# Kernel optimization log

Hardware: AMD Instinct MI355X
Metric: run time of the kernel (lower is better)

## Reference

```python
import jax, jax.numpy as jnp
import numpy as np

B_, H_, N_, L_ = 4, 512, 64, 2048  # batch, d_model, d_state/2 (conj pairs), seq len


def setup_inputs() -> dict:
    key = jax.random.key(0)
    ks = jax.random.split(key, 8)
    x = jax.random.normal(ks[0], (B_, H_, L_), jnp.float32)
    ln_w = jnp.ones((H_,), jnp.float32)
    ln_b = jnp.zeros((H_,), jnp.float32)
    # S4D-style init: dt log-uniform in [1e-3, 1e-1], A = -1/2 + i*pi*n (S4D-Lin)
    log_dt = jax.random.uniform(ks[1], (H_,), jnp.float32) * (np.log(0.1) - np.log(0.001)) + np.log(0.001)
    log_A_real = jnp.broadcast_to(jnp.log(jnp.float32(0.5)), (H_, N_))
    A_imag = jnp.broadcast_to(np.pi * jnp.arange(N_, dtype=np.float32), (H_, N_))
    B_re = jnp.ones((H_, N_), jnp.float32)
    B_im = jnp.zeros((H_, N_), jnp.float32)
    # 2 kernel channels for bidirectional
    C_re = jax.random.normal(ks[2], (2, H_, N_), jnp.float32) * (0.5 ** 0.5)
    C_im = jax.random.normal(ks[3], (2, H_, N_), jnp.float32) * (0.5 ** 0.5)
    D = jax.random.normal(ks[4], (H_,), jnp.float32)
    W_out = jax.random.normal(ks[5], (H_, H_), jnp.float32) / np.sqrt(H_)
    b_out = jnp.zeros((H_,), jnp.float32)
    return dict(x=x, ln_w=ln_w, ln_b=ln_b, log_dt=log_dt, log_A_real=log_A_real,
                A_imag=A_imag, B_re=B_re, B_im=B_im, C_re=C_re, C_im=C_im,
                D=D, W_out=W_out, b_out=b_out)


def _s4_layer(x, ln_w, ln_b, log_dt, log_A_real, A_imag, B_re, B_im, C_re, C_im, D, W_out, b_out):
    Bb, H, L = x.shape
    # ---- pre-norm LayerNorm over channel dim (module transposes to (B,L,H)) ----
    zt = x.transpose(0, 2, 1)                          # (B, L, H)
    mu = zt.mean(-1, keepdims=True)
    var = jnp.mean((zt - mu) ** 2, -1, keepdims=True)
    zt = (zt - mu) * jax.lax.rsqrt(var + 1e-5) * ln_w + ln_b
    z = zt.transpose(0, 2, 1)                          # (B, H, L)
    # ---- S4 diagonal SSM kernel, ZOH discretization, 2 channels (bidirectional) ----
    dt = jnp.exp(log_dt)[:, None]                      # (H, 1)
    A = -jnp.exp(log_A_real) + 1j * A_imag             # (H, N)
    dtA = A * dt                                       # (H, N)
    dB = (B_re + 1j * B_im) * (jnp.exp(dtA) - 1.0) / A # (H, N) discretized B
    CB = (C_re + 1j * C_im) * dB                       # (2, H, N)
    V = jnp.exp(dtA[:, :, None] * jnp.arange(L))       # (H, N, L) Vandermonde exp(l*dt*A)
    k = 2.0 * jnp.real(jnp.einsum('chn,hnl->chl', CB, V))  # (2, H, L)
    # ---- bidirectional: causal + flipped anticausal kernel, length 2L ----
    zpad = jnp.zeros_like(k[0])
    kb = jnp.concatenate([k[0], zpad], -1) + jnp.concatenate([zpad, k[1][:, ::-1]], -1)  # (H, 2L)
    # ---- FFT convolution ----
    k_f = jnp.fft.rfft(kb, n=2 * L)                    # (H, L+1)
    u_f = jnp.fft.rfft(z, n=2 * L)                     # (B, H, L+1)
    y = jnp.fft.irfft(u_f * k_f, n=2 * L)[..., :L]     # (B, H, L)
    y = y + z * D[:, None]                             # skip connection D*u
    y = jax.nn.gelu(y)                                 # default S4 activation
    y = jnp.einsum('oh,bhl->bol', W_out, y) + b_out[:, None]  # output linear (Conv1d k=1)
    return y + x                                       # residual of S4Layer


def reference(x, ln_w, ln_b, log_dt, log_A_real, A_imag, B_re, B_im, C_re, C_im, D, W_out, b_out):
    return _s4_layer(x, ln_w, ln_b, log_dt, log_A_real, A_imag, B_re, B_im, C_re, C_im, D, W_out, b_out)
```

## Files before the change

### kernel.cpp

```cpp
#include <hip/hip_runtime.h>
#include <math.h>

#define Bq 4
#define Hq 512
#define Nq 64
#define Lq 2048
#define PARAM (Hq*Nq)
#define T 64
#define NC (Lq/T)
#define NCOL 256

__global__ void prep_kernel(const float* __restrict__ log_dt,
                            const float* __restrict__ log_A_real,
                            const float* __restrict__ A_imag,
                            const float* __restrict__ B_re, const float* __restrict__ B_im,
                            const float* __restrict__ C_re, const float* __restrict__ C_im,
                            float* __restrict__ a0, float* __restrict__ b0,
                            float* __restrict__ a1, float* __restrict__ b1,
                            float* __restrict__ pw, float* __restrict__ pwT) {
    int idx = blockIdx.x * blockDim.x + threadIdx.x;
    if (idx >= PARAM) return;
    int h = idx >> 6, n = idx & 63;
    float dt = expf(log_dt[h]);
    float Ar = -expf(log_A_real[idx]);
    float Ai = A_imag[idx];
    float er = expf(Ar * dt);
    float wr = er * cosf(Ai * dt);
    float wi = er * sinf(Ai * dt);
    float mr = wr - 1.0f, mi = wi;
    float den = Ar * Ar + Ai * Ai;
    float qr = (mr * Ar + mi * Ai) / den;
    float qi = (mi * Ar - mr * Ai) / den;
    float Br = B_re[idx], Bi = B_im[idx];
    float dBr = Br * qr - Bi * qi;
    float dBi = Br * qi + Bi * qr;
    float cr = C_re[idx], ci = C_im[idx];
    a0[idx] =  2.0f * (cr * dBr - ci * dBi);
    b0[idx] = -2.0f * (cr * dBi + ci * dBr);
    cr = C_re[PARAM + idx]; ci = C_im[PARAM + idx];
    a1[idx] =  2.0f * (cr * dBr - ci * dBi);
    b1[idx] = -2.0f * (cr * dBi + ci * dBr);
    float c = 1.f, s = 0.f;
    float* base  = pw  + (size_t)h * 65 * 128 + 2 * n;
    float* baseT = pwT + (size_t)(h * 64 + n) * 132;
    for (int d = 0; d <= 64; ++d) {
        *(float2*)(base + (size_t)d * 128) = float2{c, s};
        *(float2*)(baseT + 2 * d)          = float2{c, s};
        float nc = c * wr - s * wi;
        float ns = c * wi + s * wr;
        c = nc; s = ns;
    }
}

__global__ __launch_bounds__(128)
void ktap_kernel(const float* __restrict__ pw,
                 const float* __restrict__ a0, const float* __restrict__ b0,
                 const float* __restrict__ a1, const float* __restrict__ b1,
                 float* __restrict__ kt) {
    int h = blockIdx.x;
    int t = threadIdx.x;
    int dir = t >> 6, d = t & 63;
    const float* aa = dir ? a1 : a0;
    const float* bb = dir ? b1 : b0;
    const float* row = pw + (size_t)(h * 65 + d) * 128;
    float acc = 0.f;
    for (int n = 0; n < 64; ++n) {
        float2 v = *(const float2*)(row + 2 * n);
        acc = fmaf(aa[h * 64 + n], v.x, acc);
        acc = fmaf(bb[h * 64 + n], v.y, acc);
    }
    kt[((size_t)h * 2 + dir) * 64 + d] = acc;
}

__global__ __launch_bounds__(256)
void ln_kernel(const float* __restrict__ x, const float* __restrict__ lnw,
               const float* __restrict__ lnb, float* __restrict__ z) {
    int blk = blockIdx.x;
    int b  = blk / (Lq / 16);
    int l0 = (blk % (Lq / 16)) * 16;
    int tx = threadIdx.x & 15;
    int ty = threadIdx.x >> 4;
    const float* xb = x + (size_t)b * Hq * Lq;
    float s = 0.f, s2 = 0.f;
    for (int h = ty; h < Hq; h += 16) {
        float v = xb[h * Lq + l0 + tx];
        s += v; s2 += v * v;
    }
    __shared__ float rs_[16][17], r2_[16][17], mu_s[16], sg_s[16];
    rs_[ty][tx] = s; r2_[ty][tx] = s2;
    __syncthreads();
    if (ty == 0) {
        float a = 0.f, c = 0.f;
        #pragma unroll
        for (int i = 0; i < 16; ++i) { a += rs_[i][tx]; c += r2_[i][tx]; }
        float mu = a * (1.0f / Hq);
        float var = c * (1.0f / Hq) - mu * mu;
        mu_s[tx] = mu;
        sg_s[tx] = rsqrtf(var + 1e-5f);
    }
    __syncthreads();
    float mu = mu_s[tx], rs = sg_s[tx];
    float* zb = z + (size_t)b * Hq * Lq;
    for (int h = ty; h < Hq; h += 16) {
        float v = xb[h * Lq + l0 + tx];
        zb[h * Lq + l0 + tx] = (v - mu) * rs * lnw[h] + lnb[h];
    }
}

__global__ __launch_bounds__(256, 6)
void delta_kernel(const float* __restrict__ z, const float* __restrict__ pw,
                  float* __restrict__ buf) {
    __shared__ float Bs[64][68];
    int h = blockIdx.x, ct = blockIdx.y;
    int t = threadIdx.x;
    int dir = ct >> 1;
    int cc = t & 31, rb = (t >> 5) & 1, jg = t >> 6;
    int b = (ct & 1) * 2 + rb;
    const float* zb = z + ((size_t)b * Hq + h) * Lq;
    if (dir == 0) {
        #pragma unroll
        for (int f = 0; f < 4; ++f) {
            float4 v = *(const float4*)(zb + cc * 64 + 16 * jg + 4 * f);
            Bs[16*jg+4*f+0][rb*32+cc] = v.x;
            Bs[16*jg+4*f+1][rb*32+cc] = v.y;
            Bs[16*jg+4*f+2][rb*32+cc] = v.z;
            Bs[16*jg+4*f+3][rb*32+cc] = v.w;
        }
    } else {
        #pragma unroll
        for (int f = 0; f < 4; ++f) {
            float4 v = *(const float4*)(zb + 2044 - cc * 64 - 16 * jg - 4 * f);
            Bs[16*jg+4*f+3][rb*32+cc] = v.x;
            Bs[16*jg+4*f+2][rb*32+cc] = v.y;
            Bs[16*jg+4*f+1][rb*32+cc] = v.z;
            Bs[16*jg+4*f+0][rb*32+cc] = v.w;
        }
    }
    __syncthreads();
    int tx = t & 15, ty = t >> 4;
    float aR[4][4] = {}, aI[4][4] = {};
    const float* pwh = pw + (size_t)h * 65 * 128;
    #pragma unroll 4
    for (int kk = 0; kk < 64; ++kk) {
        int d = 63 - kk;
        const float4* pr = (const float4*)(pwh + (size_t)d * 128 + 8 * tx);
        float4 p0 = pr[0], p1 = pr[1];
        float4 bv = *(const float4*)&Bs[kk][4 * ty];
        float pc[4] = {p0.x, p0.z, p1.x, p1.z};
        float ps[4] = {p0.y, p0.w, p1.y, p1.w};
        #pragma unroll
        for (int rr = 0; rr < 4; ++rr) {
            #pragma unroll
            for (int q = 0; q < 4; ++q) {
                aR[rr][q] = fmaf(pc[rr], (&bv.x)[q], aR[rr][q]);
                aI[rr][q] = fmaf(ps[rr], (&bv.x)[q], aI[rr][q]);
            }
        }
    }
    #pragma unroll
    for (int q = 0; q < 4; ++q) {
        int colg = ct * 64 + 4 * ty + q;
        float* dst = buf + ((size_t)h * NCOL + colg) * 128 + 8 * tx;
        float4 v1, v2;
        v1.x = aR[0][q]; v1.y = aI[0][q]; v1.z = aR[1][q]; v1.w = aI[1][q];
        v2.x = aR[2][q]; v2.y = aI[2][q]; v2.z = aR[3][q]; v2.w = aI[3][q];
        *(float4*)dst = v1; *(float4*)(dst + 4) = v2;
    }
}

__global__ __launch_bounds__(256)
void cscan_kernel(const float* __restrict__ pw, float* __restrict__ buf) {
    int e = blockIdx.x * 4 + (threadIdx.x >> 6);
    int n = threadIdx.x & 63;
    int h = e >> 3, dir = (e >> 2) & 1, b = e & 3;
    float2 t64 = *(const float2*)(pw + (size_t)(h * 65 + 64) * 128 + 2 * n);
    float tc = t64.x, ts = t64.y;
    float sr = 0.f, si = 0.f;
    float2* p = (float2*)(buf + ((size_t)h * NCOL + dir * 128 + b * 32) * 128) + n;
    float2 d = p[0];
    for (int c = 0; c < NC; ++c) {
        float2 dn;
        if (c + 1 < NC) dn = p[(c + 1) * 64];
        float2 s; s.x = sr; s.y = si;
        p[c * 64] = s;
        float nr = fmaf(tc, sr, fmaf(-ts, si, d.x));
        float ni = fmaf(ts, sr, fmaf(tc, si, d.y));
        sr = nr; si = ni; d = dn;
    }
}

__global__ __launch_bounds__(256, 4)
void yact_kernel(const float* __restrict__ z, const float* __restrict__ pwT,
                 const float* __restrict__ a0, const float* __restrict__ b0,
                 const float* __restrict__ a1, const float* __restrict__ b1,
                 const float* __restrict__ kt, const float* __restrict__ buf,
                 const float* __restrict__ Dv, float* __restrict__ u) {
    __shared__ float As[64][68];
    __shared__ float Bs[64][68];
    __shared__ float ks0[64], ks1[64], as0_[64], bs0_[64], as1_[64], bs1_[64];
    int h = blockIdx.x, bp = blockIdx.y;
    int t = threadIdx.x;
    if (t < 64) {
        ks0[t]  = kt[((size_t)h * 2 + 0) * 64 + t];
        ks1[t]  = kt[((size_t)h * 2 + 1) * 64 + t];
        as0_[t] = a0[h * 64 + t]; bs0_[t] = b0[h * 64 + t];
        as1_[t] = a1[h * 64 + t]; bs1_[t] = b1[h * 64 + t];
    }
    int tx = t & 15, ty = t >> 4;
    int si = t & 63, kg = t >> 6;
    int bS = 2 * bp + (si >> 5), ch = si & 31;
    const float* zb   = z + ((size_t)bS * Hq + h) * Lq + ch * 64;
    const float* bufh = buf + (size_t)h * NCOL * 128;
    const float* buf0 = bufh + (size_t)(bS * 32 + ch) * 128;
    const float* buf1 = bufh + (size_t)(128 + bS * 32 + (31 - ch)) * 128;
    const float* pwh  = pwT + (size_t)h * 64 * 132;
    float4 rB[4];
    float2 pv[8];
    #pragma unroll
    for (int f = 0; f < 4; ++f)
        rB[f] = *(const float4*)(zb + 16 * kg + 4 * f);
    float acc[4][4] = {};
    __syncthreads();
    for (int p = 0; p < 5; ++p) {
        if (p == 0) {
            #pragma unroll
            for (int q = 0; q < 16; ++q) {
                int kk = 16 * kg + q;
                int d = si - kk;
                As[kk][si] = (d >= 0) ? ks0[d] : ks1[-d - 1];
            }
        } else {
            const float* as_ = (p < 3) ? as0_ : as1_;
            const float* bs_ = (p < 3) ? bs0_ : bs1_;
            int pp = (p < 3) ? (p - 1) : (p - 3);
            #pragma unroll
            for (int q = 0; q < 16; ++q) {
                int j = q >> 1;
                int n = 32 * pp + 8 * kg + j;
                float vx = pv[j].x, vy = pv[j].y;
                As[16 * kg + q][si] = ((q & 1) == 0)
                    ? fmaf(as_[n], vx, bs_[n] * vy)
                    : fmaf(bs_[n], vx, -as_[n] * vy);
            }
        }
        #pragma unroll
        for (int f = 0; f < 4; ++f) {
            Bs[16*kg + 4*f + 0][si] = rB[f].x;
            Bs[16*kg + 4*f + 1][si] = rB[f].y;
            Bs[16*kg + 4*f + 2][si] = rB[f].z;
            Bs[16*kg + 4*f + 3][si] = rB[f].w;
        }
        __syncthreads();
        if (p < 4) {
            int pn = p + 1;
            int pp = (pn < 3) ? (pn - 1) : (pn - 3);
            const float* src = (pn < 3) ? buf0 : buf1;
            #pragma unroll
            for (int f = 0; f < 4; ++f)
                rB[f] = *(const float4*)(src + 64 * pp + 16 * kg + 4 * f);
            int dsel = (pn < 3) ? (si + 1) : (63 - si);
            #pragma unroll
            for (int j = 0; j < 8; ++j) {
                int n = 32 * pp + 8 * kg + j;
                pv[j] = *(const float2*)(pwh + (size_t)n * 132 + 2 * dsel);
            }
        }
        #pragma unroll 8
        for (int kk = 0; kk < 64; ++kk) {
            float4 av = *(const float4*)&As[kk][4 * tx];
            float4 bv = *(const float4*)&Bs[kk][4 * ty];
            #pragma unroll
            for (int ii = 0; ii < 4; ++ii) {
                float a = (&av.x)[ii];
                acc[ii][0] = fmaf(a, bv.x, acc[ii][0]);
                acc[ii][1] = fmaf(a, bv.y, acc[ii][1]);
                acc[ii][2] = fmaf(a, bv.z, acc[ii][2]);
                acc[ii][3] = fmaf(a, bv.w, acc[ii][3]);
            }
        }
        __syncthreads();
    }
    float dv = Dv[h];
    #pragma unroll
    for (int q = 0; q < 4; ++q) {
        int cc2 = 4 * ty + q;
        int b2 = 2 * bp + (cc2 >> 5), ch2 = cc2 & 31;
        size_t base = ((size_t)b2 * Hq + h) * Lq + ch2 * 64 + 4 * tx;
        float4 zr = *(const float4*)(z + base);
        float vv[4];
        vv[0] = acc[0][q] + dv * zr.x;
        vv[1] = acc[1][q] + dv * zr.y;
        vv[2] = acc[2][q] + dv * zr.z;
        vv[3] = acc[3][q] + dv * zr.w;
        #pragma unroll
        for (int i = 0; i < 4; ++i) {
            float v = vv[i];
            float tt = tanhf(0.7978845608028654f * (v + 0.044715f * v * v * v));
            vv[i] = 0.5f * v * (1.0f + tt);
        }
        float4 r; r.x = vv[0]; r.y = vv[1]; r.z = vv[2]; r.w = vv[3];
        *(float4*)(u + base) = r;
    }
}

__global__ __launch_bounds__(512, 4)
void gemm_kernel(const float* __restrict__ u, const float* __restrict__ W,
                 const float* __restrict__ bias, const float* __restrict__ x,
                 float* __restrict__ out) {
    int l0 = blockIdx.x * 64;
    int o0 = blockIdx.y * 128;
    int b  = blockIdx.z;
    int tid = threadIdx.x;
    __shared__ float Ws[2][32][132];
    __shared__ float Us[2][32][68];
    const float* ub = u + (size_t)b * Hq * Lq;
    float acc[4][4] = {};
    int wo = tid >> 4, wl = tid & 15;
    int sj = tid & 31, so = tid >> 5;
    int sl = tid & 63, sk = tid >> 6;
    float wreg[8], ureg[4];
    #pragma unroll
    for (int r = 0; r < 8; ++r) wreg[r] = W[(size_t)(o0 + so + 16*r) * Hq + sj];
    #pragma unroll
    for (int r = 0; r < 4; ++r) ureg[r] = ub[(size_t)(4*sk + r) * Lq + l0 + sl];
    #pragma unroll
    for (int r = 0; r < 8; ++r) Ws[0][sj][so + 16*r] = wreg[r];
    #pragma unroll
    for (int r = 0; r < 4; ++r) Us[0][4*sk + r][sl] = ureg[r];
    __syncthreads();
    for (int t = 0; t < Hq / 32; ++t) {
        int cur = t & 1;
        if (t < 15) {
            int k0 = (t + 1) * 32;
            #pragma unroll
            for (int r = 0; r < 8; ++r)
                wreg[r] = W[(size_t)(o0 + so + 16*r) * Hq + k0 + sj];
            #pragma unroll
            for (int r = 0; r < 4; ++r)
                ureg[r] = ub[(size_t)(k0 + 4*sk + r) * Lq + l0 + sl];
        }
        #pragma unroll 8
        for (int j = 0; j < 32; ++j) {
            float4 av = *(const float4*)&Ws[cur][j][4 * wo];
            float4 bv = *(const float4*)&Us[cur][j][4 * wl];
            #pragma unroll
            for (int io = 0; io < 4; ++io) {
                float a = (&av.x)[io];
                acc[io][0] = fmaf(a, bv.x, acc[io][0]);
                acc[io][1] = fmaf(a, bv.y, acc[io][1]);
                acc[io][2] = fmaf(a, bv.z, acc[io][2]);
                acc[io][3] = fmaf(a, bv.w, acc[io][3]);
            }
        }
        if (t < 15) {
            int nxt = cur ^ 1;
            #pragma unroll
            for (int r = 0; r < 8; ++r) Ws[nxt][sj][so + 16*r] = wreg[r];
            #pragma unroll
            for (int r = 0; r < 4; ++r) Us[nxt][4*sk + r][sl] = ureg[r];
        }
        __syncthreads();
    }
    #pragma unroll
    for (int io = 0; io < 4; ++io) {
        int o = o0 + 4 * wo + io;
        float bo = bias[o];
        size_t base = ((size_t)b * Hq + o) * Lq + l0 + 4 * wl;
        const float4 xr = *(const float4*)(x + base);
        float4 r;
        r.x = acc[io][0] + bo + xr.x;
        r.y = acc[io][1] + bo + xr.y;
        r.z = acc[io][2] + bo + xr.z;
        r.w = acc[io][3] + bo + xr.w;
        *(float4*)(out + base) = r;
    }
}

extern "C" void kernel_launch(void* const* d_in, const int* in_sizes, int n_in,
                              void* d_out, int out_size, void* d_ws, size_t ws_size,
                              hipStream_t stream) {
    (void)in_sizes; (void)n_in; (void)out_size; (void)ws_size;
    const float* x          = (const float*)d_in[0];
    const float* ln_w       = (const float*)d_in[1];
    const float* ln_b       = (const float*)d_in[2];
    const float* log_dt     = (const float*)d_in[3];
    const float* log_A_real = (const float*)d_in[4];
    const float* A_imag     = (const float*)d_in[5];
    const float* B_re       = (const float*)d_in[6];
    const float* B_im       = (const float*)d_in[7];
    const float* C_re       = (const float*)d_in[8];
    const float* C_im       = (const float*)d_in[9];
    const float* Dv         = (const float*)d_in[10];
    const float* W          = (const float*)d_in[11];
    const float* b_out      = (const float*)d_in[12];
    float* out = (float*)d_out;
    float* ws  = (float*)d_ws;

    const size_t BHL = (size_t)Bq * Hq * Lq;
    float* a0  = ws;
    float* b0  = ws + (size_t)PARAM;
    float* a1  = ws + 2 * (size_t)PARAM;
    float* b1  = ws + 3 * (size_t)PARAM;
    float* kt  = ws + 4 * (size_t)PARAM;
    float* pw  = ws + 6 * (size_t)PARAM;
    float* pwT = ws + 136 * (size_t)PARAM;
    float* z   = ws + 268 * (size_t)PARAM;
    float* u   = z  + BHL;
    float* buf = u + BHL;

    prep_kernel<<<PARAM / 256, 256, 0, stream>>>(log_dt, log_A_real, A_imag,
                                                 B_re, B_im, C_re, C_im,
                                                 a0, b0, a1, b1, pw, pwT);
    ln_kernel<<<Bq * (Lq / 16), 256, 0, stream>>>(x, ln_w, ln_b, z);
    ktap_kernel<<<Hq, 128, 0, stream>>>(pw, a0, b0, a1, b1, kt);
    delta_kernel<<<dim3(Hq, 4), 256, 0, stream>>>(z, pw, buf);
    cscan_kernel<<<Bq * Hq * 2 / 4, 256, 0, stream>>>(pw, buf);
    yact_kernel<<<dim3(Hq, 2), 256, 0, stream>>>(z, pwT, a0, b0, a1, b1,
                                                 kt, buf, Dv, u);
    gemm_kernel<<<dim3(Lq / 64, Hq / 128, Bq), 512, 0, stream>>>(u, W, b_out, x, out);
}
```

Baseline: 316.3 us.

## Restructure output GEMM to read W via wave-uniform scalar loads

The output projection GEMM changes from a 128x64 tile with both W and u staged in shared memory to a 32x128 tile where each wave owns 8 output rows. W values are wave-uniform, read through readfirstlane-indexed loads, which the compiler can turn into scalar loads, so only u is double-buffered in LDS. This removes the W shared-memory traffic and the transpose stores, at the cost of lower per-thread reuse (8x2 accumulators instead of 4x4) and more blocks.

```diff
diff --git a/kernel.cpp b/kernel.cpp
--- a/kernel.cpp
+++ b/kernel.cpp
@@ -303,76 +303,75 @@
     }
 }
 
-__global__ __launch_bounds__(512, 4)
+__global__ __launch_bounds__(256, 4)
 void gemm_kernel(const float* __restrict__ u, const float* __restrict__ W,
                  const float* __restrict__ bias, const float* __restrict__ x,
                  float* __restrict__ out) {
-    int l0 = blockIdx.x * 64;
-    int o0 = blockIdx.y * 128;
+    __shared__ float Us[2][32][128];
+    int l0 = blockIdx.x * 128;
+    int o0 = blockIdx.y * 32;
     int b  = blockIdx.z;
-    int tid = threadIdx.x;
-    __shared__ float Ws[2][32][132];
-    __shared__ float Us[2][32][68];
+    int t  = threadIdx.x;
+    int wv = __builtin_amdgcn_readfirstlane(t >> 6);
+    int ln = t & 63;
+    int ow = o0 + 8 * wv;
     const float* ub = u + (size_t)b * Hq * Lq;
-    float acc[4][4] = {};
-    int wo = tid >> 4, wl = tid & 15;
-    int sj = tid & 31, so = tid >> 5;
-    int sl = tid & 63, sk = tid >> 6;
-    float wreg[8], ureg[4];
-    #pragma unroll
-    for (int r = 0; r < 8; ++r) wreg[r] = W[(size_t)(o0 + so + 16*r) * Hq + sj];
-    #pragma unroll
-    for (int r = 0; r < 4; ++r) ureg[r] = ub[(size_t)(4*sk + r) * Lq + l0 + sl];
-    #pragma unroll
-    for (int r = 0; r < 8; ++r) Ws[0][sj][so + 16*r] = wreg[r];
-    #pragma unroll
-    for (int r = 0; r < 4; ++r) Us[0][4*sk + r][sl] = ureg[r];
+    int sf = t & 31;
+    int sk = t >> 5;
+    float4 st[4];
+    #pragma unroll
+    for (int r = 0; r < 4; ++r)
+        st[r] = *(const float4*)(ub + (size_t)(sk + 8*r) * Lq + l0 + 4*sf);
+    #pragma unroll
+    for (int r = 0; r < 4; ++r)
+        *(float4*)&Us[0][sk + 8*r][4*sf] = st[r];
     __syncthreads();
-    for (int t = 0; t < Hq / 32; ++t) {
-        int cur = t & 1;
-        if (t < 15) {
-            int k0 = (t + 1) * 32;
-            #pragma unroll
-            for (int r = 0; r < 8; ++r)
-                wreg[r] = W[(size_t)(o0 + so + 16*r) * Hq + k0 + sj];
+    float acc[8][2] = {};
+    for (int kt = 0; kt < Hq / 32; ++kt) {
+        int cur = kt & 1;
+        if (kt < 15) {
+            int k0 = (kt + 1) * 32;
             #pragma unroll
             for (int r = 0; r < 4; ++r)
-                ureg[r] = ub[(size_t)(k0 + 4*sk + r) * Lq + l0 + sl];
-        }
-        #pragma unroll 8
-        for (int j = 0; j < 32; ++j) {
-            float4 av = *(const float4*)&Ws[cur][j][4 * wo];
-            float4 bv = *(const float4*)&Us[cur][j][4 * wl];
-            #pragma unroll
-            for (int io = 0; io < 4; ++io) {
-                float a = (&av.x)[io];
-                acc[io][0] = fmaf(a, bv.x, acc[io][0]);
-                acc[io][1] = fmaf(a, bv.y, acc[io][1]);
-                acc[io][2] = fmaf(a, bv.z, acc[io][2]);
-                acc[io][3] = fmaf(a, bv.w, acc[io][3]);
-            }
-        }
-        if (t < 15) {
+                st[r] = *(const float4*)(ub + (size_t)(k0 + sk + 8*r) * Lq + l0 + 4*sf);
+        }
+        #pragma unroll
+        for (int ks = 0; ks < 4; ++ks) {
+            float ws[8][8];
+            #pragma unroll
+            for (int o = 0; o < 8; ++o) {
+                const float* wrow = W + (size_t)(ow + o) * Hq + kt * 32 + ks * 8;
+                #pragma unroll
+                for (int kk = 0; kk < 8; ++kk) ws[o][kk] = wrow[kk];
+            }
+            #pragma unroll
+            for (int kk = 0; kk < 8; ++kk) {
+                float2 uv = *(const float2*)&Us[cur][ks * 8 + kk][2 * ln];
+                #pragma unroll
+                for (int o = 0; o < 8; ++o) {
+                    acc[o][0] = fmaf(ws[o][kk], uv.x, acc[o][0]);
+                    acc[o][1] = fmaf(ws[o][kk], uv.y, acc[o][1]);
+                }
+            }
+        }
+        if (kt < 15) {
             int nxt = cur ^ 1;
             #pragma unroll
-            for (int r = 0; r < 8; ++r) Ws[nxt][sj][so + 16*r] = wreg[r];
-            #pragma unroll
-            for (int r = 0; r < 4; ++r) Us[nxt][4*sk + r][sl] = ureg[r];
+            for (int r = 0; r < 4; ++r)
+                *(float4*)&Us[nxt][sk + 8*r][4*sf] = st[r];
         }
         __syncthreads();
     }
     #pragma unroll
-    for (int io = 0; io < 4; ++io) {
-        int o = o0 + 4 * wo + io;
-        float bo = bias[o];
-        size_t base = ((size_t)b * Hq + o) * Lq + l0 + 4 * wl;
-        const float4 xr = *(const float4*)(x + base);
-        float4 r;
-        r.x = acc[io][0] + bo + xr.x;
-        r.y = acc[io][1] + bo + xr.y;
-        r.z = acc[io][2] + bo + xr.z;
-        r.w = acc[io][3] + bo + xr.w;
-        *(float4*)(out + base) = r;
+    for (int o = 0; o < 8; ++o) {
+        int oo = ow + o;
+        float bo = bias[oo];
+        size_t base = ((size_t)b * Hq + oo) * Lq + l0 + 2 * ln;
+        float2 xr = *(const float2*)(x + base);
+        float2 r;
+        r.x = acc[o][0] + bo + xr.x;
+        r.y = acc[o][1] + bo + xr.y;
+        *(float2*)(out + base) = r;
     }
 }
 
@@ -417,5 +416,5 @@
     cscan_kernel<<<Bq * Hq * 2 / 4, 256, 0, stream>>>(pw, buf);
     yact_kernel<<<dim3(Hq, 2), 256, 0, stream>>>(z, pwT, a0, b0, a1, b1,
                                                  kt, buf, Dv, u);
-    gemm_kernel<<<dim3(Lq / 64, Hq / 128, Bq), 512, 0, stream>>>(u, W, b_out, x, out);
-}
+    gemm_kernel<<<dim3(Lq / 128, Hq / 32, Bq), 256, 0, stream>>>(u, W, b_out, x, out);
+}
```

Result: slower. 386.3 us (+22.1%).

## Fuse prep/LN, ktap/delta, and chunk scan into fewer kernels

Applied to the files above, without the earlier changes.

Merges the parameter prep and LayerNorm kernels into one launch using a block-index split, and folds the kernel-tap computation into the delta kernel as an extra grid row. The chunk-carry scan now runs inside the delta kernel on its shared-memory tile, so buf is written once instead of written, reread and rewritten by a separate scan kernel. This cuts launches and global traffic on buf. In exchange the delta kernel uses more shared memory (lower occupancy bound of 3) and runs a serial scan on only 128 threads per block.

```diff
diff --git a/kernel.cpp b/kernel.cpp
--- a/kernel.cpp
+++ b/kernel.cpp
@@ -10,72 +10,54 @@
 #define NC (Lq/T)
 #define NCOL 256
 
-__global__ void prep_kernel(const float* __restrict__ log_dt,
-                            const float* __restrict__ log_A_real,
-                            const float* __restrict__ A_imag,
-                            const float* __restrict__ B_re, const float* __restrict__ B_im,
-                            const float* __restrict__ C_re, const float* __restrict__ C_im,
-                            float* __restrict__ a0, float* __restrict__ b0,
-                            float* __restrict__ a1, float* __restrict__ b1,
-                            float* __restrict__ pw, float* __restrict__ pwT) {
-    int idx = blockIdx.x * blockDim.x + threadIdx.x;
-    if (idx >= PARAM) return;
-    int h = idx >> 6, n = idx & 63;
-    float dt = expf(log_dt[h]);
-    float Ar = -expf(log_A_real[idx]);
-    float Ai = A_imag[idx];
-    float er = expf(Ar * dt);
-    float wr = er * cosf(Ai * dt);
-    float wi = er * sinf(Ai * dt);
-    float mr = wr - 1.0f, mi = wi;
-    float den = Ar * Ar + Ai * Ai;
-    float qr = (mr * Ar + mi * Ai) / den;
-    float qi = (mi * Ar - mr * Ai) / den;
-    float Br = B_re[idx], Bi = B_im[idx];
-    float dBr = Br * qr - Bi * qi;
-    float dBi = Br * qi + Bi * qr;
-    float cr = C_re[idx], ci = C_im[idx];
-    a0[idx] =  2.0f * (cr * dBr - ci * dBi);
-    b0[idx] = -2.0f * (cr * dBi + ci * dBr);
-    cr = C_re[PARAM + idx]; ci = C_im[PARAM + idx];
-    a1[idx] =  2.0f * (cr * dBr - ci * dBi);
-    b1[idx] = -2.0f * (cr * dBi + ci * dBr);
-    float c = 1.f, s = 0.f;
-    float* base  = pw  + (size_t)h * 65 * 128 + 2 * n;
-    float* baseT = pwT + (size_t)(h * 64 + n) * 132;
-    for (int d = 0; d <= 64; ++d) {
-        *(float2*)(base + (size_t)d * 128) = float2{c, s};
-        *(float2*)(baseT + 2 * d)          = float2{c, s};
-        float nc = c * wr - s * wi;
-        float ns = c * wi + s * wr;
-        c = nc; s = ns;
-    }
-}
-
-__global__ __launch_bounds__(128)
-void ktap_kernel(const float* __restrict__ pw,
-                 const float* __restrict__ a0, const float* __restrict__ b0,
-                 const float* __restrict__ a1, const float* __restrict__ b1,
-                 float* __restrict__ kt) {
-    int h = blockIdx.x;
-    int t = threadIdx.x;
-    int dir = t >> 6, d = t & 63;
-    const float* aa = dir ? a1 : a0;
-    const float* bb = dir ? b1 : b0;
-    const float* row = pw + (size_t)(h * 65 + d) * 128;
-    float acc = 0.f;
-    for (int n = 0; n < 64; ++n) {
-        float2 v = *(const float2*)(row + 2 * n);
-        acc = fmaf(aa[h * 64 + n], v.x, acc);
-        acc = fmaf(bb[h * 64 + n], v.y, acc);
-    }
-    kt[((size_t)h * 2 + dir) * 64 + d] = acc;
-}
-
 __global__ __launch_bounds__(256)
-void ln_kernel(const float* __restrict__ x, const float* __restrict__ lnw,
-               const float* __restrict__ lnb, float* __restrict__ z) {
-    int blk = blockIdx.x;
+void setup_kernel(const float* __restrict__ log_dt,
+                  const float* __restrict__ log_A_real,
+                  const float* __restrict__ A_imag,
+                  const float* __restrict__ B_re, const float* __restrict__ B_im,
+                  const float* __restrict__ C_re, const float* __restrict__ C_im,
+                  float* __restrict__ a0, float* __restrict__ b0,
+                  float* __restrict__ a1, float* __restrict__ b1,
+                  float* __restrict__ pw, float* __restrict__ pwT,
+                  const float* __restrict__ x, const float* __restrict__ lnw,
+                  const float* __restrict__ lnb, float* __restrict__ z) {
+    __shared__ float rs_[16][17], r2_[16][17], mu_s[16], sg_s[16];
+    int bx = blockIdx.x;
+    if (bx < 128) {
+        int idx = bx * 256 + threadIdx.x;
+        int h = idx >> 6, n = idx & 63;
+        float dt = expf(log_dt[h]);
+        float Ar = -expf(log_A_real[idx]);
+        float Ai = A_imag[idx];
+        float er = expf(Ar * dt);
+        float wr = er * cosf(Ai * dt);
+        float wi = er * sinf(Ai * dt);
+        float mr = wr - 1.0f, mi = wi;
+        float den = Ar * Ar + Ai * Ai;
+        float qr = (mr * Ar + mi * Ai) / den;
+        float qi = (mi * Ar - mr * Ai) / den;
+        float Br = B_re[idx], Bi = B_im[idx];
+        float dBr = Br * qr - Bi * qi;
+        float dBi = Br * qi + Bi * qr;
+        float cr = C_re[idx], ci = C_im[idx];
+        a0[idx] =  2.0f * (cr * dBr - ci * dBi);
+        b0[idx] = -2.0f * (cr * dBi + ci * dBr);
+        cr = C_re[PARAM + idx]; ci = C_im[PARAM + idx];
+        a1[idx] =  2.0f * (cr * dBr - ci * dBi);
+        b1[idx] = -2.0f * (cr * dBi + ci * dBr);
+        float c = 1.f, s = 0.f;
+        float* base  = pw  + (size_t)h * 65 * 128 + 2 * n;
+        float* baseT = pwT + (size_t)(h * 64 + n) * 132;
+        for (int d = 0; d <= 64; ++d) {
+            *(float2*)(base + (size_t)d * 128) = float2{c, s};
+            *(float2*)(baseT + 2 * d)          = float2{c, s};
+            float nc = c * wr - s * wi;
+            float ns = c * wi + s * wr;
+            c = nc; s = ns;
+        }
+        return;
+    }
+    int blk = bx - 128;
     int b  = blk / (Lq / 16);
     int l0 = (blk % (Lq / 16)) * 16;
     int tx = threadIdx.x & 15;
@@ -86,7 +68,6 @@
         float v = xb[h * Lq + l0 + tx];
         s += v; s2 += v * v;
     }
-    __shared__ float rs_[16][17], r2_[16][17], mu_s[16], sg_s[16];
     rs_[ty][tx] = s; r2_[ty][tx] = s2;
     __syncthreads();
     if (ty == 0) {
@@ -107,12 +88,32 @@
     }
 }
 
-__global__ __launch_bounds__(256, 6)
-void delta_kernel(const float* __restrict__ z, const float* __restrict__ pw,
-                  float* __restrict__ buf) {
+__global__ __launch_bounds__(256, 3)
+void deltascan_kernel(const float* __restrict__ z, const float* __restrict__ pw,
+                      const float* __restrict__ a0, const float* __restrict__ b0,
+                      const float* __restrict__ a1, const float* __restrict__ b1,
+                      float* __restrict__ kt, float* __restrict__ buf) {
     __shared__ float Bs[64][68];
-    int h = blockIdx.x, ct = blockIdx.y;
+    __shared__ float Ds[64][130];
+    int h = blockIdx.x;
     int t = threadIdx.x;
+    if (blockIdx.y == 4) {
+        if (t < 128) {
+            int dir = t >> 6, d = t & 63;
+            const float* aa = dir ? a1 : a0;
+            const float* bb = dir ? b1 : b0;
+            const float* row = pw + (size_t)(h * 65 + d) * 128;
+            float acc = 0.f;
+            for (int n = 0; n < 64; ++n) {
+                float2 v = *(const float2*)(row + 2 * n);
+                acc = fmaf(aa[h * 64 + n], v.x, acc);
+                acc = fmaf(bb[h * 64 + n], v.y, acc);
+            }
+            kt[((size_t)h * 2 + dir) * 64 + d] = acc;
+        }
+        return;
+    }
+    int ct = blockIdx.y;
     int dir = ct >> 1;
     int cc = t & 31, rb = (t >> 5) & 1, jg = t >> 6;
     int b = (ct & 1) * 2 + rb;
@@ -159,34 +160,35 @@
     }
     #pragma unroll
     for (int q = 0; q < 4; ++q) {
-        int colg = ct * 64 + 4 * ty + q;
-        float* dst = buf + ((size_t)h * NCOL + colg) * 128 + 8 * tx;
+        float* dst = &Ds[4 * ty + q][8 * tx];
         float4 v1, v2;
         v1.x = aR[0][q]; v1.y = aI[0][q]; v1.z = aR[1][q]; v1.w = aI[1][q];
         v2.x = aR[2][q]; v2.y = aI[2][q]; v2.z = aR[3][q]; v2.w = aI[3][q];
         *(float4*)dst = v1; *(float4*)(dst + 4) = v2;
     }
-}
-
-__global__ __launch_bounds__(256)
-void cscan_kernel(const float* __restrict__ pw, float* __restrict__ buf) {
-    int e = blockIdx.x * 4 + (threadIdx.x >> 6);
-    int n = threadIdx.x & 63;
-    int h = e >> 3, dir = (e >> 2) & 1, b = e & 3;
-    float2 t64 = *(const float2*)(pw + (size_t)(h * 65 + 64) * 128 + 2 * n);
-    float tc = t64.x, ts = t64.y;
-    float sr = 0.f, si = 0.f;
-    float2* p = (float2*)(buf + ((size_t)h * NCOL + dir * 128 + b * 32) * 128) + n;
-    float2 d = p[0];
-    for (int c = 0; c < NC; ++c) {
-        float2 dn;
-        if (c + 1 < NC) dn = p[(c + 1) * 64];
-        float2 s; s.x = sr; s.y = si;
-        p[c * 64] = s;
-        float nr = fmaf(tc, sr, fmaf(-ts, si, d.x));
-        float ni = fmaf(ts, sr, fmaf(tc, si, d.y));
-        sr = nr; si = ni; d = dn;
-    }
+    __syncthreads();
+    if (t < 128) {
+        int bl = t >> 6, n = t & 63;
+        float2 w64 = *(const float2*)(pw + (size_t)(h * 65 + 64) * 128 + 2 * n);
+        float tc = w64.x, ts = w64.y;
+        float sr = 0.f, si = 0.f;
+        #pragma unroll 4
+        for (int c = 0; c < NC; ++c) {
+            int col = bl * 32 + c;
+            float dr = Ds[col][2 * n], di = Ds[col][2 * n + 1];
+            Ds[col][2 * n] = sr; Ds[col][2 * n + 1] = si;
+            float nr = fmaf(tc, sr, fmaf(-ts, si, dr));
+            float ni = fmaf(ts, sr, fmaf(tc, si, di));
+            sr = nr; si = ni;
+        }
+    }
+    __syncthreads();
+    int colo = t >> 2, qg = t & 3;
+    const float* srcd = &Ds[colo][qg * 32];
+    float* dstg = buf + ((size_t)h * NCOL + ct * 64 + colo) * 128 + qg * 32;
+    #pragma unroll
+    for (int f = 0; f < 8; ++f)
+        *(float4*)(dstg + 4 * f) = *(const float4*)(srcd + 4 * f);
 }
 
 __global__ __launch_bounds__(256, 4)
@@ -232,11 +234,10 @@
         } else {
             const float* as_ = (p < 3) ? as0_ : as1_;
             const float* bs_ = (p < 3) ? bs0_ : bs1_;
-            int pp = (p < 3) ? (p - 1) : (p - 3);
             #pragma unroll
             for (int q = 0; q < 16; ++q) {
                 int j = q >> 1;
-                int n = 32 * pp + 8 * kg + j;
+                int n = 32 * ((p < 3) ? (p - 1) : (p - 3)) + 8 * kg + j;
                 float vx = pv[j].x, vy = pv[j].y;
                 As[16 * kg + q][si] = ((q & 1) == 0)
                     ? fmaf(as_[n], vx, bs_[n] * vy)
@@ -408,13 +409,11 @@
     float* u   = z  + BHL;
     float* buf = u + BHL;
 
-    prep_kernel<<<PARAM / 256, 256, 0, stream>>>(log_dt, log_A_real, A_imag,
-                                                 B_re, B_im, C_re, C_im,
-                                                 a0, b0, a1, b1, pw, pwT);
-    ln_kernel<<<Bq * (Lq / 16), 256, 0, stream>>>(x, ln_w, ln_b, z);
-    ktap_kernel<<<Hq, 128, 0, stream>>>(pw, a0, b0, a1, b1, kt);
-    delta_kernel<<<dim3(Hq, 4), 256, 0, stream>>>(z, pw, buf);
-    cscan_kernel<<<Bq * Hq * 2 / 4, 256, 0, stream>>>(pw, buf);
+    setup_kernel<<<128 + Bq * (Lq / 16), 256, 0, stream>>>(
+        log_dt, log_A_real, A_imag, B_re, B_im, C_re, C_im,
+        a0, b0, a1, b1, pw, pwT, x, ln_w, ln_b, z);
+    deltascan_kernel<<<dim3(Hq, 5), 256, 0, stream>>>(z, pw, a0, b0, a1, b1,
+                                                      kt, buf);
     yact_kernel<<<dim3(Hq, 2), 256, 0, stream>>>(z, pwT, a0, b0, a1, b1,
                                                  kt, buf, Dv, u);
     gemm_kernel<<<dim3(Lq / 64, Hq / 128, Bq), 512, 0, stream>>>(u, W, b_out, x, out);
```

Result: faster. 299.4 us (-5.3%).
